# Optimization experiments

Measured on AMD Instinct MI355X. Metric: run time of the kernel, lower is better.

## Reference

```python
import jax, jax.numpy as jnp
import numpy as np

H = 64        # gru_hiddens
HEADS = 4     # n_heads
HID = 64      # n_hidden (is_concat=False -> out_features)
RT = 4        # role_types
APT = 3       # agents per type
N_AMB = 1023  # ambiguous agents; N = 1 + N_AMB = 1024
SLOPE = 0.2


def _leaky(x):
    return jnp.where(x >= 0, x, SLOPE * x)


def _linear(x, W, b):
    return x @ W.T + b


def setup_inputs() -> dict:
    key = jax.random.key(0)
    ks = jax.random.split(key, 18)
    s = 0.1
    return {
        "hidden": jax.random.normal(ks[0], (1, H), jnp.float32),
        "ambiguous": jax.random.normal(ks[1], (N_AMB, H), jnp.float32),
        "type_agents": jax.random.normal(ks[2], (RT, APT, 1, H), jnp.float32),
        # per-role-type routing MLPs and merge/self MLPs
        "W_self": jax.random.normal(ks[3], (H, H), jnp.float32) * s,
        "b_self": jnp.zeros((H,), jnp.float32),
        "W_merge": jax.random.normal(ks[4], (H, 2 * H), jnp.float32) * s,
        "b_merge": jnp.zeros((H,), jnp.float32),
        "W_trans": jax.random.normal(ks[5], (RT, H, H), jnp.float32) * s,
        "b_trans": jnp.zeros((RT, H), jnp.float32),
        # GATv2 params (no biases)
        "W_l": jax.random.normal(ks[6], (HEADS * HID, H), jnp.float32) * s,
        "W_r": jax.random.normal(ks[7], (HEADS * HID, H), jnp.float32) * s,
        "w_attn": jax.random.normal(ks[8], (HID,), jnp.float32) * s,
        # type_define MLP: 2H -> 64 -> 128 -> RT
        "Wd0": jax.random.normal(ks[9], (64, 2 * H), jnp.float32) * s,
        "bd0": jnp.zeros((64,), jnp.float32),
        "Wd1": jax.random.normal(ks[10], (128, 64), jnp.float32) * s,
        "bd1": jnp.zeros((128,), jnp.float32),
        "Wd2": jax.random.normal(ks[11], (RT, 128), jnp.float32) * s,
        "bd2": jnp.zeros((RT,), jnp.float32),
    }


def reference(hidden, ambiguous, type_agents,
              W_self, b_self, W_merge, b_merge, W_trans, b_trans,
              W_l, W_r, w_attn,
              Wd0, bd0, Wd1, bd1, Wd2, bd2):
    # per-role-type routing + merge
    hidden_1 = _linear(hidden, W_self, b_self)  # [1, H]
    for t in range(RT):
        # mean over agents of trans_mlp[t](agent)
        tmp = (jnp.einsum('aih,oh->aio', type_agents[t], W_trans[t]) + b_trans[t]).mean(axis=0)
        hidden_1 = _leaky(_linear(jnp.concatenate([hidden_1, tmp], axis=-1), W_merge, b_merge))

    h = jnp.concatenate([hidden_1, ambiguous], axis=0)  # [N, H], N = 1 + N_AMB
    n = h.shape[0]

    # GATv2 dense pairwise attention (adjacency all-True; dropout in eval = identity)
    g_l = (h @ W_l.T).reshape(n, HEADS, HID)
    g_r = (h @ W_r.T).reshape(n, HEADS, HID)
    # g_sum[i, j] = g_l[j] + g_r[i]  -> [N, N, HEADS, HID]
    g_sum = g_l[None, :, :, :] + g_r[:, None, :, :]
    e = jnp.einsum('ijhf,f->ijh', _leaky(g_sum), w_attn)  # [N, N, HEADS]
    a = jax.nn.softmax(e, axis=1)
    attn_res = jnp.einsum('ijh,jhf->ihf', a, g_r)  # [N, HEADS, HID]
    gat_out = attn_res.mean(axis=1)  # is_concat=False -> mean over heads, [N, HID]

    hidden_2 = gat_out[0]  # [HID]
    rep = jnp.broadcast_to(hidden_2[None, :], (ambiguous.shape[0], HID))
    x = jnp.concatenate([ambiguous, rep], axis=-1)  # [N_AMB, 2H]
    x = _leaky(_linear(x, Wd0, bd0))
    x = _leaky(_linear(x, Wd1, bd1))
    x = _linear(x, Wd2, bd2)
    return jax.nn.sigmoid(x)  # [N_AMB, RT]
```

## Files before the change

kernel.cpp:

```cpp
#include <hip/hip_runtime.h>
#include <math.h>

#define SLOPE 0.2f
#define KA_BLK 256
#define KA_ROWS 4
#define PART_STRIDE 320

__device__ __forceinline__ float leaky(float x) { return x >= 0.f ? x : SLOPE * x; }


__global__ __launch_bounds__(256) void kA_gat(
    const float* __restrict__ hidden, const float* __restrict__ ambiguous,
    const float* __restrict__ type_agents,
    const float* __restrict__ W_self, const float* __restrict__ b_self,
    const float* __restrict__ W_merge, const float* __restrict__ b_merge,
    const float* __restrict__ W_trans, const float* __restrict__ b_trans,
    const float* __restrict__ W_l, const float* __restrict__ W_r,
    const float* __restrict__ w_attn, float* __restrict__ ws)
{
    __shared__ __align__(16) float tmean[4][64];
    __shared__ __align__(16) float tmpv[4][64];
    __shared__ __align__(16) float hstage[64];
    __shared__ __align__(16) float h1[64];
    __shared__ __align__(16) float hrow[KA_ROWS][64];

    const int t = threadIdx.x;
    const int o = t & 63;
    const int r = t >> 6;
    const int b = blockIdx.x;

    float4 wr[16], wl[16];
    {
        const float4* Wr4 = (const float4*)(W_r + t * 64);
        const float4* Wl4 = (const float4*)(W_l + t * 64);
#pragma unroll
        for (int k = 0; k < 16; k++) { wr[k] = Wr4[k]; wl[k] = Wl4[k]; }
    }

    float hv = 0.f;
    if (r == 0) {
        float acc = b_self[o];
        const float4* w4 = (const float4*)(W_self + o * 64);
#pragma unroll
        for (int k = 0; k < 16; k++) {
            float4 w = w4[k];
            acc += w.x * hidden[k*4+0] + w.y * hidden[k*4+1]
                 + w.z * hidden[k*4+2] + w.w * hidden[k*4+3];
        }
        hv = acc;
    }

    tmean[r][o] = (type_agents[r*192 + o] + type_agents[r*192 + 64 + o]
                 + type_agents[r*192 + 128 + o]) * (1.f / 3.f);
    __threadfence_block();
    {
        float tv = b_trans[r*64 + o];
        const float4* w4 = (const float4*)(W_trans + r*4096 + o*64);
        const float4* tm4 = (const float4*)(&tmean[r][0]);
#pragma unroll
        for (int k = 0; k < 16; k++) {
            float4 w = w4[k]; float4 m = tm4[k];
            tv += w.x*m.x + w.y*m.y + w.z*m.z + w.w*m.w;
        }
        tmpv[r][o] = tv;
    }

    if (r != 0) {
        int u = t - 64;
#pragma unroll
        for (int i = 0; i < 2; i++) {
            int idx = u + 192 * i;
            if (idx < KA_ROWS * 64) {
                int rl = idx >> 6, c = idx & 63;
                int j = b * KA_ROWS + rl;
                hrow[rl][c] = (j == 0) ? 0.f : ambiguous[(j - 1) * 64 + c];
            }
        }
    }
    __syncthreads();

    if (r == 0) {
        const float4* w4 = (const float4*)(W_merge + o * 128);
        for (int tt = 0; tt < 4; tt++) {
            hstage[o] = hv;
            __threadfence_block();
            float acc = b_merge[o];
            const float4* hs4 = (const float4*)(&hstage[0]);
            const float4* tp4 = (const float4*)(&tmpv[tt][0]);
#pragma unroll
            for (int k = 0; k < 16; k++) {
                float4 w = w4[k];        float4 v = hs4[k];
                acc += w.x*v.x + w.y*v.y + w.z*v.z + w.w*v.w;
                float4 w2 = w4[16 + k];  float4 u = tp4[k];
                acc += w2.x*u.x + w2.y*u.y + w2.z*u.z + w2.w*u.w;
            }
            hv = leaky(acc);
            __threadfence_block();
        }
        h1[o] = hv;
    }
    __syncthreads();

    if (b == 0 && t < 64) hrow[0][o] = h1[o];

    float g0 = 0.f;
#pragma unroll
    for (int k = 0; k < 16; k++) {
        float4 w = wr[k];
        g0 += w.x * h1[k*4+0] + w.y * h1[k*4+1] + w.z * h1[k*4+2] + w.w * h1[k*4+3];
    }
    __syncthreads();

    float accl[KA_ROWS], accr[KA_ROWS];
#pragma unroll
    for (int rr = 0; rr < KA_ROWS; rr++) { accl[rr] = 0.f; accr[rr] = 0.f; }
#pragma unroll
    for (int kk = 0; kk < 16; kk++) {
        float4 a = wl[kk];
        float4 c = wr[kk];
#pragma unroll
        for (int rr = 0; rr < KA_ROWS; rr++) {
            float x0 = hrow[rr][kk*4+0], x1 = hrow[rr][kk*4+1];
            float x2 = hrow[rr][kk*4+2], x3 = hrow[rr][kk*4+3];
            accl[rr] += a.x*x0 + a.y*x1 + a.z*x2 + a.w*x3;
            accr[rr] += c.x*x0 + c.y*x1 + c.z*x2 + c.w*x3;
        }
    }

    const float wa = w_attn[o];
    float numsum = 0.f, denp = 0.f;
#pragma unroll
    for (int rr = 0; rr < KA_ROWS; rr++) {
        float ec = leaky(accl[rr] + g0) * wa;
#pragma unroll
        for (int off = 32; off; off >>= 1) ec += __shfl_xor(ec, off, 64);
        float w = expf(ec);
        numsum += w * accr[rr];
        denp   += w;
    }
    ws[b * PART_STRIDE + t] = numsum;
    if (o == 0) ws[b * PART_STRIDE + 256 + r] = denp;
}

__global__ __launch_bounds__(256) void kB_mlp(
    const float* __restrict__ ambiguous,
    const float* __restrict__ Wd0, const float* __restrict__ bd0,
    const float* __restrict__ Wd1, const float* __restrict__ bd1,
    const float* __restrict__ Wd2, const float* __restrict__ bd2,
    const float* __restrict__ ws, float* __restrict__ out)
{
    __shared__ __align__(16) float x[4][128];
    __shared__ __align__(16) float y0[4][64];
    __shared__ __align__(16) float y1[4][128];
    __shared__ __align__(16) float hs[4][64];
    const int t  = threadIdx.x;
    const int o  = t & 63;
    const int r  = t >> 6;
    const int r0 = blockIdx.x * 4;

    {
        int row = r0 + r;
        x[r][o] = (row < 1023) ? ambiguous[row * 64 + o] : 0.f;
    }

    float nsum = 0.f;
#pragma unroll 16
    for (int bb = 0; bb < KA_BLK; bb++) nsum += ws[bb * PART_STRIDE + t];

    float d = ws[o * PART_STRIDE + 256 + r]
            + ws[(o + 64)  * PART_STRIDE + 256 + r]
            + ws[(o + 128) * PART_STRIDE + 256 + r]
            + ws[(o + 192) * PART_STRIDE + 256 + r];
#pragma unroll
    for (int off = 32; off; off >>= 1) d += __shfl_xor(d, off, 64);
    hs[r][o] = nsum / d;
    __syncthreads();
    if (t < 64) {
        float h2 = 0.25f * (hs[0][o] + hs[1][o] + hs[2][o] + hs[3][o]);
        x[0][64 + o] = h2; x[1][64 + o] = h2; x[2][64 + o] = h2; x[3][64 + o] = h2;
    }
    __syncthreads();

    {
        float acc = bd0[o];
        const float4* w4 = (const float4*)(Wd0 + o * 128);
        const float4* xr = (const float4*)(&x[r][0]);
#pragma unroll
        for (int kk = 0; kk < 32; kk++) {
            float4 w = w4[kk]; float4 xv = xr[kk];
            acc += w.x*xv.x + w.y*xv.y + w.z*xv.z + w.w*xv.w;
        }
        y0[r][o] = leaky(acc);
    }
    __syncthreads();

#pragma unroll
    for (int rep = 0; rep < 2; rep++) {
        int idx = rep * 256 + t;
        int rr = idx >> 7, oo = idx & 127;
        float acc = bd1[oo];
        const float4* w4 = (const float4*)(Wd1 + oo * 64);
        const float4* yr = (const float4*)(&y0[rr][0]);
#pragma unroll
        for (int kk = 0; kk < 16; kk++) {
            float4 w = w4[kk]; float4 yv = yr[kk];
            acc += w.x*yv.x + w.y*yv.y + w.z*yv.z + w.w*yv.w;
        }
        y1[rr][oo] = leaky(acc);
    }
    __syncthreads();

    if (t < 16) {
        int rr = t >> 2, c = t & 3;
        int row = r0 + rr;
        if (row < 1023) {
            float acc = bd2[c];
            const float4* w4 = (const float4*)(Wd2 + c * 128);
            const float4* yr = (const float4*)(&y1[rr][0]);
#pragma unroll
            for (int kk = 0; kk < 32; kk++) {
                float4 w = w4[kk]; float4 yv = yr[kk];
                acc += w.x*yv.x + w.y*yv.y + w.z*yv.z + w.w*yv.w;
            }
            out[row * 4 + c] = 1.f / (1.f + expf(-acc));
        }
    }
}

extern "C" void kernel_launch(void* const* d_in, const int* in_sizes, int n_in,
                              void* d_out, int out_size, void* d_ws, size_t ws_size,
                              hipStream_t stream)
{
    const float* hidden      = (const float*)d_in[0];
    const float* ambiguous   = (const float*)d_in[1];
    const float* type_agents = (const float*)d_in[2];
    const float* W_self      = (const float*)d_in[3];
    const float* b_self      = (const float*)d_in[4];
    const float* W_merge     = (const float*)d_in[5];
    const float* b_merge     = (const float*)d_in[6];
    const float* W_trans     = (const float*)d_in[7];
    const float* b_trans     = (const float*)d_in[8];
    const float* W_l         = (const float*)d_in[9];
    const float* W_r         = (const float*)d_in[10];
    const float* w_attn      = (const float*)d_in[11];
    const float* Wd0         = (const float*)d_in[12];
    const float* bd0         = (const float*)d_in[13];
    const float* Wd1         = (const float*)d_in[14];
    const float* bd1         = (const float*)d_in[15];
    const float* Wd2         = (const float*)d_in[16];
    const float* bd2         = (const float*)d_in[17];
    float* ws  = (float*)d_ws;
    float* out = (float*)d_out;

    kA_gat<<<KA_BLK, 256, 0, stream>>>(hidden, ambiguous, type_agents,
                                       W_self, b_self, W_merge, b_merge,
                                       W_trans, b_trans, W_l, W_r, w_attn, ws);
    kB_mlp<<<256, 256, 0, stream>>>(ambiguous, Wd0, bd0, Wd1, bd1, Wd2, bd2, ws, out);
}
```

Baseline: 123.9 us.

## Move partial-sum reduction into a separate kernel and process 8 rows per MLP block

Previously every MLP block redundantly reduced all 256 GAT partial numerators and denominators. A small 4-block kernel now performs that reduction once and writes the per-head result into workspace, and the MLP kernel just reads 256 values. The MLP kernel also handles 8 rows per block across 128 blocks instead of 4 rows across 256, so weight loads are reused over more rows. This adds a third kernel launch and a workspace dependency between kernels.

```diff
diff --git a/kernel.cpp b/kernel.cpp
--- a/kernel.cpp
+++ b/kernel.cpp
@@ -5,6 +5,9 @@
 #define KA_BLK 256
 #define KA_ROWS 4
 #define PART_STRIDE 320
+#define HS_BASE (KA_BLK * PART_STRIDE)
+#define KB_BLK 128
+#define KB_ROWS 8
 
 __device__ __forceinline__ float leaky(float x) { return x >= 0.f ? x : SLOPE * x; }
 
@@ -142,6 +145,36 @@
     if (o == 0) ws[b * PART_STRIDE + 256 + r] = denp;
 }
 
+__global__ __launch_bounds__(256) void kR_reduce(float* ws)
+{
+    __shared__ float part[4][64];
+    __shared__ float dsh[4];
+    const int t = threadIdx.x;
+    const int o = t & 63;
+    const int c = t >> 6;
+    const int h = blockIdx.x;
+
+    float s = 0.f;
+#pragma unroll 8
+    for (int i = 0; i < 64; i++) {
+        int bb = c * 64 + i;
+        s += ws[bb * PART_STRIDE + h * 64 + o];
+    }
+    part[c][o] = s;
+
+    float d = ws[t * PART_STRIDE + 256 + h];
+#pragma unroll
+    for (int off = 32; off; off >>= 1) d += __shfl_xor(d, off, 64);
+    if (o == 0) dsh[c] = d;
+    __syncthreads();
+
+    if (t < 64) {
+        float num = part[0][o] + part[1][o] + part[2][o] + part[3][o];
+        float den = dsh[0] + dsh[1] + dsh[2] + dsh[3];
+        ws[HS_BASE + h * 64 + o] = num / den;
+    }
+}
+
 __global__ __launch_bounds__(256) void kB_mlp(
     const float* __restrict__ ambiguous,
     const float* __restrict__ Wd0, const float* __restrict__ bd0,
@@ -149,74 +182,67 @@
     const float* __restrict__ Wd2, const float* __restrict__ bd2,
     const float* __restrict__ ws, float* __restrict__ out)
 {
-    __shared__ __align__(16) float x[4][128];
-    __shared__ __align__(16) float y0[4][64];
-    __shared__ __align__(16) float y1[4][128];
-    __shared__ __align__(16) float hs[4][64];
+    __shared__ __align__(16) float x[KB_ROWS][128];
+    __shared__ __align__(16) float y0[KB_ROWS][64];
+    __shared__ __align__(16) float y1[KB_ROWS][128];
     const int t  = threadIdx.x;
     const int o  = t & 63;
-    const int r  = t >> 6;
-    const int r0 = blockIdx.x * 4;
-
-    {
-        int row = r0 + r;
-        x[r][o] = (row < 1023) ? ambiguous[row * 64 + o] : 0.f;
-    }
-
-    float nsum = 0.f;
-#pragma unroll 16
-    for (int bb = 0; bb < KA_BLK; bb++) nsum += ws[bb * PART_STRIDE + t];
-
-    float d = ws[o * PART_STRIDE + 256 + r]
-            + ws[(o + 64)  * PART_STRIDE + 256 + r]
-            + ws[(o + 128) * PART_STRIDE + 256 + r]
-            + ws[(o + 192) * PART_STRIDE + 256 + r];
-#pragma unroll
-    for (int off = 32; off; off >>= 1) d += __shfl_xor(d, off, 64);
-    hs[r][o] = nsum / d;
-    __syncthreads();
+    const int r0 = blockIdx.x * KB_ROWS;
+
+#pragma unroll
+    for (int i = 0; i < 2; i++) {
+        int idx = t + 256 * i;
+        int rl = idx >> 6, c = idx & 63;
+        int row = r0 + rl;
+        x[rl][c] = (row < 1023) ? ambiguous[row * 64 + c] : 0.f;
+    }
     if (t < 64) {
-        float h2 = 0.25f * (hs[0][o] + hs[1][o] + hs[2][o] + hs[3][o]);
-        x[0][64 + o] = h2; x[1][64 + o] = h2; x[2][64 + o] = h2; x[3][64 + o] = h2;
-    }
-    __syncthreads();
-
-    {
-        float acc = bd0[o];
-        const float4* w4 = (const float4*)(Wd0 + o * 128);
-        const float4* xr = (const float4*)(&x[r][0]);
+        float h2 = 0.25f * (ws[HS_BASE + o]       + ws[HS_BASE + 64 + o]
+                          + ws[HS_BASE + 128 + o] + ws[HS_BASE + 192 + o]);
+#pragma unroll
+        for (int rl = 0; rl < KB_ROWS; rl++) x[rl][64 + o] = h2;
+    }
+    __syncthreads();
+
+#pragma unroll
+    for (int i = 0; i < 2; i++) {
+        int idx = t + 256 * i;
+        int rl = idx >> 6, c = idx & 63;
+        float acc = bd0[c];
+        const float4* w4 = (const float4*)(Wd0 + c * 128);
+        const float4* xr = (const float4*)(&x[rl][0]);
 #pragma unroll
         for (int kk = 0; kk < 32; kk++) {
             float4 w = w4[kk]; float4 xv = xr[kk];
             acc += w.x*xv.x + w.y*xv.y + w.z*xv.z + w.w*xv.w;
         }
-        y0[r][o] = leaky(acc);
-    }
-    __syncthreads();
-
-#pragma unroll
-    for (int rep = 0; rep < 2; rep++) {
-        int idx = rep * 256 + t;
-        int rr = idx >> 7, oo = idx & 127;
-        float acc = bd1[oo];
-        const float4* w4 = (const float4*)(Wd1 + oo * 64);
-        const float4* yr = (const float4*)(&y0[rr][0]);
+        y0[rl][c] = leaky(acc);
+    }
+    __syncthreads();
+
+#pragma unroll
+    for (int i = 0; i < 4; i++) {
+        int idx = t + 256 * i;
+        int rl = idx >> 7, c = idx & 127;
+        float acc = bd1[c];
+        const float4* w4 = (const float4*)(Wd1 + c * 64);
+        const float4* yr = (const float4*)(&y0[rl][0]);
 #pragma unroll
         for (int kk = 0; kk < 16; kk++) {
             float4 w = w4[kk]; float4 yv = yr[kk];
             acc += w.x*yv.x + w.y*yv.y + w.z*yv.z + w.w*yv.w;
         }
-        y1[rr][oo] = leaky(acc);
-    }
-    __syncthreads();
-
-    if (t < 16) {
-        int rr = t >> 2, c = t & 3;
-        int row = r0 + rr;
+        y1[rl][c] = leaky(acc);
+    }
+    __syncthreads();
+
+    if (t < 32) {
+        int rl = t >> 2, c = t & 3;
+        int row = r0 + rl;
         if (row < 1023) {
             float acc = bd2[c];
             const float4* w4 = (const float4*)(Wd2 + c * 128);
-            const float4* yr = (const float4*)(&y1[rr][0]);
+            const float4* yr = (const float4*)(&y1[rl][0]);
 #pragma unroll
             for (int kk = 0; kk < 32; kk++) {
                 float4 w = w4[kk]; float4 yv = yr[kk];
@@ -255,5 +281,6 @@
     kA_gat<<<KA_BLK, 256, 0, stream>>>(hidden, ambiguous, type_agents,
                                        W_self, b_self, W_merge, b_merge,
                                        W_trans, b_trans, W_l, W_r, w_attn, ws);
-    kB_mlp<<<256, 256, 0, stream>>>(ambiguous, Wd0, bd0, Wd1, bd1, Wd2, bd2, ws, out);
-}
+    kR_reduce<<<4, 256, 0, stream>>>(ws);
+    kB_mlp<<<KB_BLK, 256, 0, stream>>>(ambiguous, Wd0, bd0, Wd1, bd1, Wd2, bd2, ws, out);
+}
```

Result: slower. 127.3 us (+2.7%).
